# Kernel tuning notes

Measured on AMD Instinct MI355X. Metric: run time of the kernel, lower is better.

Reference implementation:

```python
import jax, jax.numpy as jnp
import numpy as np

B, S, D = 4, 2048, 512
H = 8
HD = D // H  # 64


def setup_inputs() -> dict:
    key = jax.random.key(0)
    k1, k2, k3 = jax.random.split(key, 3)
    x = jax.random.normal(k1, (B, S, D), dtype=jnp.float32)
    w_qkv = jax.random.normal(k2, (3 * D, D), dtype=jnp.float32) * (D ** -0.5)
    w_out = jax.random.normal(k3, (D, D), dtype=jnp.float32) * (D ** -0.5)
    return {"x": x, "w_qkv": w_qkv, "w_out": w_out}


def reference(x, w_qkv, w_out):
    b, s, d = x.shape
    # qkv projection (no bias), split into q,k,v
    qkv = jnp.einsum('bsd,ed->bse', x, w_qkv)  # [b, s, 3*d]
    q, k, v = jnp.split(qkv, 3, axis=2)
    # [b, s, h*hd] -> [b, h, s, hd]
    def to_heads(t):
        return t.reshape(b, s, H, HD).transpose(0, 2, 1, 3)
    q, k, v = to_heads(q), to_heads(k), to_heads(v)
    # NOTE: original module only scales by sqrt(head_dim) when mask is given;
    # with mask=None softmax is over raw QK^T scores.
    scores = jnp.einsum('bnid,bnjd->bnij', q, k)  # [b, h, s, s]
    attn = jax.nn.softmax(scores, axis=-1)
    o = jnp.einsum('bnij,bnjd->bnid', attn, v)  # [b, h, s, hd]
    o = o.transpose(0, 2, 1, 3).reshape(b, s, d)
    # dropout is identity (eval / drop_prob=0)
    return jnp.einsum('bsd,ed->bse', o, w_out)
```

## Files before the change

### kernel.cpp

```cpp
#include <hip/hip_runtime.h>
#include <hip/hip_bf16.h>

constexpr int B_  = 4;
constexpr int S_  = 2048;
constexpr int D_  = 512;
constexpr int H_  = 8;
constexpr int HD_ = 64;
constexpr int M_  = B_ * S_;

constexpr float LOG2E = 1.4426950408889634f;

typedef __attribute__((ext_vector_type(8))) short short8v;
typedef __attribute__((ext_vector_type(8))) _Float16 half8v;
typedef __attribute__((ext_vector_type(8))) unsigned short ushort8v;
typedef __attribute__((ext_vector_type(4))) float float4v;
typedef __attribute__((ext_vector_type(16))) float float16v;

__device__ __forceinline__ unsigned short f2bf(float x) {
    unsigned u = __builtin_bit_cast(unsigned, x);
    u += 0x7fffu + ((u >> 16) & 1u);
    return (unsigned short)(u >> 16);
}
__device__ __forceinline__ float bf2f(unsigned short h) {
    return __builtin_bit_cast(float, ((unsigned)h) << 16);
}
__device__ __forceinline__ unsigned short f2h(float x) {
    return __builtin_bit_cast(unsigned short, (_Float16)x);
}
__device__ __forceinline__ float fast_exp2(float x) {
#if __has_builtin(__builtin_amdgcn_exp2f)
    return __builtin_amdgcn_exp2f(x);
#else
    return exp2f(x);
#endif
}
__device__ __forceinline__ unsigned pack_bf16_trunc(float lo, float hi) {
    const unsigned ulo = __builtin_bit_cast(unsigned, lo);
    const unsigned uhi = __builtin_bit_cast(unsigned, hi);
#if __has_builtin(__builtin_amdgcn_perm)
    return __builtin_amdgcn_perm(uhi, ulo, 0x07060302u);
#else
    return (uhi & 0xffff0000u) | (ulo >> 16);
#endif
}
__device__ __forceinline__ void gload_lds16(const void* g, void* lds) {
    __builtin_amdgcn_global_load_lds((const __attribute__((address_space(1))) unsigned*)g,
                                     (__attribute__((address_space(3))) unsigned*)lds, 16, 0, 0);
}

__global__ __launch_bounds__(256) void prepass(const float* __restrict__ x,
                                               const float* __restrict__ wqkv,
                                               const float* __restrict__ wout,
                                               unsigned short* __restrict__ Xp,
                                               unsigned short* __restrict__ Wh,
                                               unsigned short* __restrict__ Wlq,
                                               unsigned short* __restrict__ Wob) {
    const int bid = blockIdx.x, t = threadIdx.x;
    if (bid < 2048) {
        const int flat = bid * 256 + t;
        const int m = flat >> 6, c = (flat & 63) * 8;
        const float4 a = *(const float4*)&x[(size_t)m * 512 + c];
        const float4 b = *(const float4*)&x[(size_t)m * 512 + c + 4];
        const float v[8] = {a.x, a.y, a.z, a.w, b.x, b.y, b.z, b.w};
        ushort8v hi, lo;
#pragma unroll
        for (int i = 0; i < 8; ++i) {
            const unsigned short h = f2bf(v[i]);
            hi[i] = h; lo[i] = f2bf(v[i] - bf2f(h));
        }
        *(ushort8v*)&Xp[(size_t)m * 1024 + c]       = hi;
        *(ushort8v*)&Xp[(size_t)m * 1024 + 512 + c] = lo;
    } else if (bid < 2048 + 384) {
        const int flat = (bid - 2048) * 256 + t;
        const int e = flat >> 6, c = (flat & 63) * 8;
        const float4 a = *(const float4*)&wqkv[(size_t)e * 512 + c];
        const float4 b = *(const float4*)&wqkv[(size_t)e * 512 + c + 4];
        const float v[8] = {a.x, a.y, a.z, a.w, b.x, b.y, b.z, b.w};
        ushort8v hi, lo;
#pragma unroll
        for (int i = 0; i < 8; ++i) {
            const unsigned short h = f2bf(v[i]);
            hi[i] = h; lo[i] = f2bf(v[i] - bf2f(h));
        }
        *(ushort8v*)&Wh[(size_t)e * 512 + c] = hi;
        if (e < 512) *(ushort8v*)&Wlq[(size_t)e * 512 + c] = lo;
    } else {
        const int flat = (bid - 2432) * 256 + t;
        const int e = flat >> 6, c = (flat & 63) * 8;
        const float4 a = *(const float4*)&wout[(size_t)e * 512 + c];
        const float4 b = *(const float4*)&wout[(size_t)e * 512 + c + 4];
        const float v[8] = {a.x, a.y, a.z, a.w, b.x, b.y, b.z, b.w};
        ushort8v hi;
#pragma unroll
        for (int i = 0; i < 8; ++i) hi[i] = f2bf(v[i]);
        *(ushort8v*)&Wob[(size_t)e * 512 + c] = hi;
    }
}

__global__ __launch_bounds__(256, 3) void gemm_qkv(const unsigned short* __restrict__ Xp,
                                                   const unsigned short* __restrict__ Wh,
                                                   const unsigned short* __restrict__ Wlq,
                                                   unsigned short* __restrict__ Qf,
                                                   unsigned short* __restrict__ KH,
                                                   unsigned short* __restrict__ VT) {
    __shared__ unsigned short Asm[2][128 * 64];
    __shared__ unsigned short Bsm[2][64 * 64];
    const int t = threadIdx.x, wv = t >> 6, lane = t & 63;
    const int fm = lane & 15, fq = lane >> 4;
    const int bid0 = blockIdx.x + 24 * blockIdx.y;
    const int xcd = bid0 & 7, ii = bid0 >> 3;
    const int x  = ii % 24;
    const int m0 = ((ii / 24) * 8 + xcd) * 128;
    const int slice = x >> 3;
    const int e0 = (x & 7) * 64;
    const bool vblk = (slice == 2);
    const int kiters = (slice == 0) ? 24 : 8;
    const int wrow = (wv >> 1) * 64, wcol = (wv & 1) * 32;

    const unsigned short* BbaseWh =
        Wh + (size_t)(e0 + (slice == 1 ? 512 : (slice == 2 ? 1024 : 0))) * 512;
    const unsigned short* BbaseWlq = Wlq + (size_t)e0 * 512;

    const int srow = t >> 3;
    const int skb0 = t & 7;

    float4v acc[4][2];
#pragma unroll
    for (int i = 0; i < 4; ++i)
#pragma unroll
        for (int j = 0; j < 2; ++j) acc[i][j] = (float4v){0.f, 0.f, 0.f, 0.f};

    {
#pragma unroll
        for (int i = 0; i < 4; ++i) {
            const int row = srow + 32 * i;
            const int kb = skb0 ^ (row & 7);
            gload_lds16(Xp + (size_t)(m0 + row) * 1024 + kb * 8,
                        &Asm[0][(wv * 64 + 256 * i) * 8]);
        }
#pragma unroll
        for (int i = 0; i < 2; ++i) {
            const int row = srow + 32 * i;
            const int kb = skb0 ^ (row & 7);
            gload_lds16(BbaseWh + (size_t)row * 512 + kb * 8,
                        &Bsm[0][(wv * 64 + 256 * i) * 8]);
        }
    }

    for (int kk = 0; kk < kiters; ++kk) {
        __syncthreads();

        if (kk + 1 < kiters) {
            const int nk = kk + 1;
            const int pass = nk >> 3;
            const int k0n = (nk & 7) * 64;
            const int nbuf = nk & 1;
            const int aoff = (slice == 0 && pass == 1) ? 512 : 0;
            const unsigned short* Bp = (slice == 0 && pass == 2) ? BbaseWlq : BbaseWh;
#pragma unroll
            for (int i = 0; i < 4; ++i) {
                const int row = srow + 32 * i;
                const int kb = skb0 ^ (row & 7);
                gload_lds16(Xp + (size_t)(m0 + row) * 1024 + aoff + k0n + kb * 8,
                            &Asm[nbuf][(wv * 64 + 256 * i) * 8]);
            }
#pragma unroll
            for (int i = 0; i < 2; ++i) {
                const int row = srow + 32 * i;
                const int kb = skb0 ^ (row & 7);
                gload_lds16(Bp + (size_t)row * 512 + k0n + kb * 8,
                            &Bsm[nbuf][(wv * 64 + 256 * i) * 8]);
            }
        }

        const int buf = kk & 1;
#pragma unroll
        for (int ks = 0; ks < 2; ++ks) {
            short8v af[4], bf[2];
#pragma unroll
            for (int mt = 0; mt < 4; ++mt) {
                const int row = wrow + mt * 16 + fm;
                af[mt] = *(const short8v*)&Asm[buf][row * 64 + 8 * ((4 * ks + fq) ^ (row & 7))];
            }
#pragma unroll
            for (int nt = 0; nt < 2; ++nt) {
                const int row = wcol + nt * 16 + fm;
                bf[nt] = *(const short8v*)&Bsm[buf][row * 64 + 8 * ((4 * ks + fq) ^ (row & 7))];
            }
            if (vblk) {
#pragma unroll
                for (int mt = 0; mt < 4; ++mt)
#pragma unroll
                    for (int nt = 0; nt < 2; ++nt)
                        acc[mt][nt] = __builtin_amdgcn_mfma_f32_16x16x32_bf16(bf[nt], af[mt], acc[mt][nt], 0, 0, 0);
            } else {
#pragma unroll
                for (int mt = 0; mt < 4; ++mt)
#pragma unroll
                    for (int nt = 0; nt < 2; ++nt)
                        acc[mt][nt] = __builtin_amdgcn_mfma_f32_16x16x32_bf16(af[mt], bf[nt], acc[mt][nt], 0, 0, 0);
            }
        }
    }

    if (!vblk) {
        unsigned short* __restrict__ dst = (slice == 0) ? Qf : KH;
        const float sc = (slice == 0) ? LOG2E : 1.0f;
#pragma unroll
        for (int mt = 0; mt < 4; ++mt)
#pragma unroll
            for (int nt = 0; nt < 2; ++nt) {
                const int e = e0 + wcol + nt * 16 + fm;
                const int h = e >> 6, hd = e & 63;
#pragma unroll
                for (int r = 0; r < 4; ++r) {
                    const int m = m0 + wrow + mt * 16 + 4 * fq + r;
                    const int b = m >> 11, s = m & 2047;
                    dst[((size_t)(b * 8 + h) * 2048 + s) * 64 + hd] =
                        f2h(acc[mt][nt][r] * sc);
                }
            }
    } else {
#pragma unroll
        for (int nt = 0; nt < 2; ++nt)
#pragma unroll
            for (int r = 0; r < 4; ++r) {
                const int e = e0 + wcol + nt * 16 + 4 * fq + r;
                const int h = e >> 6, hd = e & 63;
#pragma unroll
                for (int mt = 0; mt < 4; ++mt) {
                    const int m = m0 + wrow + mt * 16 + fm;
                    const int b = m >> 11, s = m & 2047;
                    const int s2 = (s & ~12) | ((s & 4) << 1) | ((s & 8) >> 1);
                    VT[((size_t)(b * 8 + h) * 64 + hd) * 2048 + s2] = f2bf(acc[mt][nt][r]);
                }
            }
    }
}

__global__ __launch_bounds__(256, 2) void attn(const unsigned short* __restrict__ Qfp,
                                               const unsigned short* __restrict__ KHp,
                                               const unsigned short* __restrict__ VTp,
                                               float* __restrict__ Op0,
                                               float* __restrict__ Op1,
                                               float* __restrict__ Lp0,
                                               float* __restrict__ Lp1) {
    __shared__ unsigned short Ks[2][64 * 64];
    __shared__ unsigned short Vs[2][64 * 64];
    const int t = threadIdx.x, wv = t >> 6, lane = t & 63;
    const int lq = lane & 31;
    const int hf2 = lane >> 5;
    const int bid0 = blockIdx.x + 32 * blockIdx.y;
    const int xcd = bid0 & 7, ii = bid0 >> 3;
    const int bh = (ii >> 5) * 8 + xcd;
    const int rr = ii & 31;
    const int q0 = (rr >> 1) * 128;
    const int jh = rr & 1;
    const int jb0 = jh * 16;

    const unsigned short* qfp = Qfp + (size_t)bh * S_ * 64;
    const unsigned short* kh  = KHp + (size_t)bh * S_ * 64;
    const unsigned short* vt  = VTp + (size_t)bh * 64 * S_;
    float* __restrict__ Op = (jh ? Op1 : Op0);
    float* __restrict__ Lp = (jh ? Lp1 : Lp0);

    const int srow = t >> 3;
    const int skb0 = t & 7;

#define STAGE_K(N, B) do {                                                      \
    _Pragma("unroll")                                                           \
    for (int i_ = 0; i_ < 2; ++i_) {                                            \
        const int row_ = srow + 32 * i_;                                        \
        const int kb_ = skb0 ^ (row_ & 7);                                      \
        gload_lds16(kh + (size_t)((N) * 64 + row_) * 64 + kb_ * 8,              \
                    &Ks[B][(wv * 64 + 256 * i_) * 8]);                          \
    } } while (0)

#define STAGE_V(N, B) do {                                                      \
    _Pragma("unroll")                                                           \
    for (int i_ = 0; i_ < 2; ++i_) {                                            \
        const int row_ = srow + 32 * i_;                                        \
        const int kb_ = skb0 ^ (row_ & 7);                                      \
        gload_lds16(vt + (size_t)row_ * S_ + (N) * 64 + kb_ * 8,                \
                    &Vs[B][(wv * 64 + 256 * i_) * 8]);                          \
    } } while (0)

#define QK_STEP(SN, KR) do {                                                    \
    _Pragma("unroll")                                                           \
    for (int jb_ = 0; jb_ < 2; ++jb_)                                           \
        _Pragma("unroll")                                                       \
        for (int r_ = 0; r_ < 16; ++r_) SN[jb_][r_] = 0.f;                      \
    _Pragma("unroll")                                                           \
    for (int kk_ = 0; kk_ < 4; ++kk_)                                           \
        _Pragma("unroll")                                                       \
        for (int jb_ = 0; jb_ < 2; ++jb_) {                                     \
            const int row_ = jb_ * 32 + lq;                                     \
            const int cb_ = 2 * kk_ + hf2;                                      \
            const half8v kf_ = *(const half8v*)&Ks[KR][row_ * 64 + 8 * (cb_ ^ (row_ & 7))]; \
            SN[jb_] = __builtin_amdgcn_mfma_f32_32x32x16_f16(kf_, qf[kk_], SN[jb_], 0, 0, 0); \
        } } while (0)

#define SOFTMAX_PV(SC, VR) do {                                                 \
    unsigned pk_[2][4][2];                                                      \
    _Pragma("unroll")                                                           \
    for (int jb_ = 0; jb_ < 2; ++jb_)                                           \
        _Pragma("unroll")                                                       \
        for (int g_ = 0; g_ < 4; ++g_) {                                        \
            const float p0_ = fast_exp2(SC[jb_][4 * g_ + 0]);                   \
            const float p1_ = fast_exp2(SC[jb_][4 * g_ + 1]);                   \
            const float p2_ = fast_exp2(SC[jb_][4 * g_ + 2]);                   \
            const float p3_ = fast_exp2(SC[jb_][4 * g_ + 3]);                   \
            lsum += (p0_ + p1_) + (p2_ + p3_);                                  \
            pk_[jb_][g_][0] = pack_bf16_trunc(p0_, p1_);                        \
            pk_[jb_][g_][1] = pack_bf16_trunc(p2_, p3_);                        \
        }                                                                       \
    __builtin_amdgcn_s_setprio(1);                                              \
    _Pragma("unroll")                                                           \
    for (int jc_ = 0; jc_ < 4; ++jc_) {                                         \
        const int jb_ = jc_ >> 1, gg_ = (jc_ & 1) * 2;                          \
        const uint4 uu_ = {pk_[jb_][gg_][0], pk_[jb_][gg_][1],                  \
                           pk_[jb_][gg_ + 1][0], pk_[jb_][gg_ + 1][1]};         \
        const short8v pa_ = __builtin_bit_cast(short8v, uu_);                   \
        _Pragma("unroll")                                                       \
        for (int db_ = 0; db_ < 2; ++db_) {                                     \
            const int vrow_ = db_ * 32 + lq;                                    \
            const int cb_ = 2 * jc_ + hf2;                                      \
            const short8v vf_ = *(const short8v*)&Vs[VR][vrow_ * 64 + 8 * (cb_ ^ (vrow_ & 7))]; \
            accO[db_] = __builtin_amdgcn_mfma_f32_32x32x16_bf16(pa_, vf_, accO[db_], 0, 0, 0);  \
        }                                                                       \
    }                                                                           \
    __builtin_amdgcn_s_setprio(0);                                              \
} while (0)

    STAGE_K(jb0, 0);
    STAGE_V(jb0, 0);
    STAGE_K(jb0 + 1, 1);

    half8v qf[4];
    {
        const int qrow = q0 + wv * 32 + lq;
#pragma unroll
        for (int kk = 0; kk < 4; ++kk)
            qf[kk] = *(const half8v*)&qfp[(size_t)qrow * 64 + kk * 16 + hf2 * 8];
    }

    float16v accO[2];
#pragma unroll
    for (int db = 0; db < 2; ++db)
#pragma unroll
        for (int r = 0; r < 16; ++r) accO[db][r] = 0.f;
    float lsum = 0.f;

    float16v sA[2], sB[2];

    __syncthreads();
    QK_STEP(sA, 0);
    __syncthreads();

    for (int n = 0; n < 16; n += 2) {
        if (n + 2 < 16) STAGE_K(jb0 + n + 2, 0);
        STAGE_V(jb0 + n + 1, 1);
        QK_STEP(sB, 1);
        SOFTMAX_PV(sA, 0);
        __syncthreads();
        if (n + 3 < 16) STAGE_K(jb0 + n + 3, 1);
        if (n + 2 < 16) {
            STAGE_V(jb0 + n + 2, 0);
            QK_STEP(sA, 0);
        }
        SOFTMAX_PV(sB, 1);
        __syncthreads();
    }

#undef STAGE_K
#undef STAGE_V
#undef QK_STEP
#undef SOFTMAX_PV

    const float ls = lsum + __shfl_xor(lsum, 32);
    if (hf2 == 0) Lp[((size_t)bh << 11) + q0 + wv * 32 + lq] = ls;

    float* op = Op + ((size_t)bh * 2048 + q0 + wv * 32) * 64;
#pragma unroll
    for (int g = 0; g < 4; ++g)
#pragma unroll
        for (int r = 0; r < 4; ++r) {
            const int qrow = r + 8 * g + 4 * hf2;
#pragma unroll
            for (int db = 0; db < 2; ++db)
                op[(size_t)qrow * 64 + db * 32 + lq] = accO[db][4 * g + r];
        }
}

__global__ __launch_bounds__(256) void combine(const float* __restrict__ Op0,
                                               const float* __restrict__ Op1,
                                               const float* __restrict__ Lp0,
                                               const float* __restrict__ Lp1,
                                               unsigned short* __restrict__ OB) {
    const size_t idx = ((size_t)blockIdx.x * 256 + threadIdx.x) * 8;
    const int bh = (int)(idx >> 17);
    const int rem = (int)(idx & 131071);
    const int q = rem >> 6, d0 = rem & 63;
    const size_t lidx = ((size_t)bh << 11) + q;
    const float inv = 1.f / (Lp0[lidx] + Lp1[lidx]);
    const float4 a0 = *(const float4*)&Op0[idx];
    const float4 a1 = *(const float4*)&Op0[idx + 4];
    const float4 b0 = *(const float4*)&Op1[idx];
    const float4 b1 = *(const float4*)&Op1[idx + 4];
    const float v[8] = {a0.x + b0.x, a0.y + b0.y, a0.z + b0.z, a0.w + b0.w,
                        a1.x + b1.x, a1.y + b1.y, a1.z + b1.z, a1.w + b1.w};
    ushort8v o;
#pragma unroll
    for (int i = 0; i < 8; ++i) o[i] = f2bf(v[i] * inv);
    const int b = bh >> 3, h = bh & 7;
    *(ushort8v*)&OB[((size_t)(b * 2048 + q)) * 512 + h * 64 + d0] = o;
}

__global__ __launch_bounds__(256) void gemm_out(const unsigned short* __restrict__ OB,
                                                const unsigned short* __restrict__ Wob,
                                                float* __restrict__ out) {
    __shared__ unsigned short Asm[2][128 * 64];
    __shared__ unsigned short Bsm[2][64 * 64];
    const int t = threadIdx.x, wv = t >> 6, lane = t & 63;
    const int fm = lane & 15, fq = lane >> 4;
    const int bid0 = blockIdx.x + 8 * blockIdx.y;
    const int xcd = bid0 & 7, ii = bid0 >> 3;
    const int e0 = (ii % 8) * 64;
    const int m0 = ((ii / 8) * 8 + xcd) * 128;
    const int wrow = (wv & 1) * 64, wcol = (wv >> 1) * 32;

    const int srow = t >> 3;
    const int skb0 = t & 7;

    float4v acc[4][2];
#pragma unroll
    for (int i = 0; i < 4; ++i)
#pragma unroll
        for (int j = 0; j < 2; ++j) acc[i][j] = (float4v){0.f, 0.f, 0.f, 0.f};

#pragma unroll
    for (int i = 0; i < 4; ++i) {
        const int row = srow + 32 * i;
        const int kb = skb0 ^ (row & 7);
        gload_lds16(OB + (size_t)(m0 + row) * 512 + kb * 8,
                    &Asm[0][(wv * 64 + 256 * i) * 8]);
    }
#pragma unroll
    for (int i = 0; i < 2; ++i) {
        const int row = srow + 32 * i;
        const int kb = skb0 ^ (row & 7);
        gload_lds16(Wob + (size_t)(e0 + row) * 512 + kb * 8,
                    &Bsm[0][(wv * 64 + 256 * i) * 8]);
    }

    for (int kk = 0; kk < 8; ++kk) {
        __syncthreads();
        if (kk + 1 < 8) {
            const int k0n = (kk + 1) * 64, nbuf = (kk + 1) & 1;
#pragma unroll
            for (int i = 0; i < 4; ++i) {
                const int row = srow + 32 * i;
                const int kb = skb0 ^ (row & 7);
                gload_lds16(OB + (size_t)(m0 + row) * 512 + k0n + kb * 8,
                            &Asm[nbuf][(wv * 64 + 256 * i) * 8]);
            }
#pragma unroll
            for (int i = 0; i < 2; ++i) {
                const int row = srow + 32 * i;
                const int kb = skb0 ^ (row & 7);
                gload_lds16(Wob + (size_t)(e0 + row) * 512 + k0n + kb * 8,
                            &Bsm[nbuf][(wv * 64 + 256 * i) * 8]);
            }
        }
        const int buf = kk & 1;
#pragma unroll
        for (int ks = 0; ks < 2; ++ks) {
            short8v af[4], bf[2];
#pragma unroll
            for (int mt = 0; mt < 4; ++mt) {
                const int row = wrow + mt * 16 + fm;
                af[mt] = *(const short8v*)&Asm[buf][row * 64 + 8 * ((4 * ks + fq) ^ (row & 7))];
            }
#pragma unroll
            for (int nt = 0; nt < 2; ++nt) {
                const int row = wcol + nt * 16 + fm;
                bf[nt] = *(const short8v*)&Bsm[buf][row * 64 + 8 * ((4 * ks + fq) ^ (row & 7))];
            }
#pragma unroll
            for (int mt = 0; mt < 4; ++mt)
#pragma unroll
                for (int nt = 0; nt < 2; ++nt)
                    acc[mt][nt] = __builtin_amdgcn_mfma_f32_16x16x32_bf16(af[mt], bf[nt], acc[mt][nt], 0, 0, 0);
        }
    }
#pragma unroll
    for (int mt = 0; mt < 4; ++mt)
#pragma unroll
        for (int nt = 0; nt < 2; ++nt)
#pragma unroll
            for (int r = 0; r < 4; ++r) {
                const int m = m0 + wrow + mt * 16 + 4 * fq + r;
                const int e = e0 + wcol + nt * 16 + fm;
                out[(size_t)m * 512 + e] = acc[mt][nt][r];
            }
}

extern "C" void kernel_launch(void* const* d_in, const int* in_sizes, int n_in,
                              void* d_out, int out_size, void* d_ws, size_t ws_size,
                              hipStream_t stream) {
    const float* x     = (const float*)d_in[0];
    const float* w_qkv = (const float*)d_in[1];
    const float* w_out = (const float*)d_in[2];
    float* out = (float*)d_out;

    char* p = (char*)d_ws;
    unsigned short* Xp  = (unsigned short*)p;  p += (size_t)M_ * 1024 * 2;
    unsigned short* Wh  = (unsigned short*)p;  p += (size_t)1536 * 512 * 2;
    unsigned short* Wlq = (unsigned short*)p;  p += (size_t)512 * 512 * 2;
    unsigned short* Wob = (unsigned short*)p;  p += (size_t)512 * 512 * 2;
    unsigned short* Qf  = (unsigned short*)p;  p += (size_t)32 * S_ * 64 * 2;
    unsigned short* KH  = (unsigned short*)p;  p += (size_t)32 * S_ * 64 * 2;
    unsigned short* VT  = (unsigned short*)p;  p += (size_t)32 * 64 * S_ * 2;
    float* Op1          = (float*)p;           p += (size_t)32 * S_ * 64 * 4;
    float* Op0 = (float*)Xp;
    float* Lp0 = (float*)Wh;
    float* Lp1 = Lp0 + (size_t)32 * S_;
    unsigned short* OB = Qf;

    prepass<<<2560, 256, 0, stream>>>(x, w_qkv, w_out, Xp, Wh, Wlq, Wob);
    gemm_qkv<<<dim3(24, 64), 256, 0, stream>>>(Xp, Wh, Wlq, Qf, KH, VT);
    attn<<<dim3(32, 32), 256, 0, stream>>>(Qf, KH, VT, Op0, Op1, Lp0, Lp1);
    combine<<<2048, 256, 0, stream>>>(Op0, Op1, Lp0, Lp1, OB);
    gemm_out<<<dim3(8, 64), 256, 0, stream>>>(OB, Wob, out);
}
```

Before: 169.3 us.

## Simplify attention loop to single-stage pipeline and raise occupancy to 3 blocks

Replaces the software-pipelined loop, which overlapped QK of the next tile with softmax/PV of the current one using two score register sets, with a simple double-buffered loop that processes each 64-key tile in two 32-column halves. This frees score registers, and launch bounds are raised to 3 blocks per CU so hardware occupancy can hide latency instead. The trade-off is losing explicit MFMA/VALU overlap within a wave, plus possible register spills under the tighter budget.

Result: no change. 172.1 us (+1.6%).

```diff
diff --git a/kernel.cpp b/kernel.cpp
--- a/kernel.cpp
+++ b/kernel.cpp
@@ -238,7 +238,7 @@
     }
 }
 
-__global__ __launch_bounds__(256, 2) void attn(const unsigned short* __restrict__ Qfp,
+__global__ __launch_bounds__(256, 3) void attn(const unsigned short* __restrict__ Qfp,
                                                const unsigned short* __restrict__ KHp,
                                                const unsigned short* __restrict__ VTp,
                                                float* __restrict__ Op0,
@@ -285,56 +285,8 @@
                     &Vs[B][(wv * 64 + 256 * i_) * 8]);                          \
     } } while (0)
 
-#define QK_STEP(SN, KR) do {                                                    \
-    _Pragma("unroll")                                                           \
-    for (int jb_ = 0; jb_ < 2; ++jb_)                                           \
-        _Pragma("unroll")                                                       \
-        for (int r_ = 0; r_ < 16; ++r_) SN[jb_][r_] = 0.f;                      \
-    _Pragma("unroll")                                                           \
-    for (int kk_ = 0; kk_ < 4; ++kk_)                                           \
-        _Pragma("unroll")                                                       \
-        for (int jb_ = 0; jb_ < 2; ++jb_) {                                     \
-            const int row_ = jb_ * 32 + lq;                                     \
-            const int cb_ = 2 * kk_ + hf2;                                      \
-            const half8v kf_ = *(const half8v*)&Ks[KR][row_ * 64 + 8 * (cb_ ^ (row_ & 7))]; \
-            SN[jb_] = __builtin_amdgcn_mfma_f32_32x32x16_f16(kf_, qf[kk_], SN[jb_], 0, 0, 0); \
-        } } while (0)
-
-#define SOFTMAX_PV(SC, VR) do {                                                 \
-    unsigned pk_[2][4][2];                                                      \
-    _Pragma("unroll")                                                           \
-    for (int jb_ = 0; jb_ < 2; ++jb_)                                           \
-        _Pragma("unroll")                                                       \
-        for (int g_ = 0; g_ < 4; ++g_) {                                        \
-            const float p0_ = fast_exp2(SC[jb_][4 * g_ + 0]);                   \
-            const float p1_ = fast_exp2(SC[jb_][4 * g_ + 1]);                   \
-            const float p2_ = fast_exp2(SC[jb_][4 * g_ + 2]);                   \
-            const float p3_ = fast_exp2(SC[jb_][4 * g_ + 3]);                   \
-            lsum += (p0_ + p1_) + (p2_ + p3_);                                  \
-            pk_[jb_][g_][0] = pack_bf16_trunc(p0_, p1_);                        \
-            pk_[jb_][g_][1] = pack_bf16_trunc(p2_, p3_);                        \
-        }                                                                       \
-    __builtin_amdgcn_s_setprio(1);                                              \
-    _Pragma("unroll")                                                           \
-    for (int jc_ = 0; jc_ < 4; ++jc_) {                                         \
-        const int jb_ = jc_ >> 1, gg_ = (jc_ & 1) * 2;                          \
-        const uint4 uu_ = {pk_[jb_][gg_][0], pk_[jb_][gg_][1],                  \
-                           pk_[jb_][gg_ + 1][0], pk_[jb_][gg_ + 1][1]};         \
-        const short8v pa_ = __builtin_bit_cast(short8v, uu_);                   \
-        _Pragma("unroll")                                                       \
-        for (int db_ = 0; db_ < 2; ++db_) {                                     \
-            const int vrow_ = db_ * 32 + lq;                                    \
-            const int cb_ = 2 * jc_ + hf2;                                      \
-            const short8v vf_ = *(const short8v*)&Vs[VR][vrow_ * 64 + 8 * (cb_ ^ (vrow_ & 7))]; \
-            accO[db_] = __builtin_amdgcn_mfma_f32_32x32x16_bf16(pa_, vf_, accO[db_], 0, 0, 0);  \
-        }                                                                       \
-    }                                                                           \
-    __builtin_amdgcn_s_setprio(0);                                              \
-} while (0)
-
     STAGE_K(jb0, 0);
     STAGE_V(jb0, 0);
-    STAGE_K(jb0 + 1, 1);
 
     half8v qf[4];
     {
@@ -351,31 +303,64 @@
         for (int r = 0; r < 16; ++r) accO[db][r] = 0.f;
     float lsum = 0.f;
 
-    float16v sA[2], sB[2];
-
     __syncthreads();
-    QK_STEP(sA, 0);
-    __syncthreads();
-
-    for (int n = 0; n < 16; n += 2) {
-        if (n + 2 < 16) STAGE_K(jb0 + n + 2, 0);
-        STAGE_V(jb0 + n + 1, 1);
-        QK_STEP(sB, 1);
-        SOFTMAX_PV(sA, 0);
-        __syncthreads();
-        if (n + 3 < 16) STAGE_K(jb0 + n + 3, 1);
-        if (n + 2 < 16) {
-            STAGE_V(jb0 + n + 2, 0);
-            QK_STEP(sA, 0);
-        }
-        SOFTMAX_PV(sB, 1);
+
+    for (int n = 0; n < 16; ++n) {
+        const int buf = n & 1;
+        if (n + 1 < 16) {
+            STAGE_K(jb0 + n + 1, buf ^ 1);
+            STAGE_V(jb0 + n + 1, buf ^ 1);
+        }
+
+#pragma unroll
+        for (int jb = 0; jb < 2; ++jb) {
+            float16v sS;
+#pragma unroll
+            for (int r = 0; r < 16; ++r) sS[r] = 0.f;
+            __builtin_amdgcn_s_setprio(1);
+#pragma unroll
+            for (int kk = 0; kk < 4; ++kk) {
+                const int row = jb * 32 + lq;
+                const int cb = 2 * kk + hf2;
+                const half8v kf = *(const half8v*)&Ks[buf][row * 64 + 8 * (cb ^ (row & 7))];
+                sS = __builtin_amdgcn_mfma_f32_32x32x16_f16(kf, qf[kk], sS, 0, 0, 0);
+            }
+            __builtin_amdgcn_s_setprio(0);
+
+            unsigned pk[4][2];
+#pragma unroll
+            for (int g = 0; g < 4; ++g) {
+                const float p0 = fast_exp2(sS[4 * g + 0]);
+                const float p1 = fast_exp2(sS[4 * g + 1]);
+                const float p2 = fast_exp2(sS[4 * g + 2]);
+                const float p3 = fast_exp2(sS[4 * g + 3]);
+                lsum += (p0 + p1) + (p2 + p3);
+                pk[g][0] = pack_bf16_trunc(p0, p1);
+                pk[g][1] = pack_bf16_trunc(p2, p3);
+            }
+
+            __builtin_amdgcn_s_setprio(1);
+#pragma unroll
+            for (int jh2 = 0; jh2 < 2; ++jh2) {
+                const int jc = jb * 2 + jh2, gg = jh2 * 2;
+                const uint4 uu = {pk[gg][0], pk[gg][1], pk[gg + 1][0], pk[gg + 1][1]};
+                const short8v pa = __builtin_bit_cast(short8v, uu);
+#pragma unroll
+                for (int db = 0; db < 2; ++db) {
+                    const int vrow = db * 32 + lq;
+                    const int cb = 2 * jc + hf2;
+                    const short8v vf = *(const short8v*)&Vs[buf][vrow * 64 + 8 * (cb ^ (vrow & 7))];
+                    accO[db] = __builtin_amdgcn_mfma_f32_32x32x16_bf16(pa, vf, accO[db], 0, 0, 0);
+                }
+            }
+            __builtin_amdgcn_s_setprio(0);
+        }
+
         __syncthreads();
     }
 
 #undef STAGE_K
 #undef STAGE_V
-#undef QK_STEP
-#undef SOFTMAX_PV
 
     const float ls = lsum + __shfl_xor(lsum, 32);
     if (hf2 == 0) Lp[((size_t)bh << 11) + q0 + wv * 32 + lq] = ls;
```
